# Performance work log

Hardware: AMD Instinct MI355X
Metric: run time of the kernel (lower is better)

## Reference

```python
import jax, jax.numpy as jnp
import numpy as np

N = 50000      # total nodes (25 graphs x 2000 proteins)
E = 1200000    # total edges
G = 25         # graphs
F_IN = 128     # protein_features
H = 64         # hidden_dim
L = 2          # num_layers


def setup_inputs() -> dict:
    key = jax.random.key(0)
    ks = jax.random.split(key, 24)
    inp = {
        "x": jax.random.normal(ks[0], (N, F_IN), dtype=jnp.float32),
        "edge_attr": jax.random.uniform(ks[1], (E,), dtype=jnp.float32),
        "global_features": jax.random.normal(ks[2], (G, 6), dtype=jnp.float32),
        "edge_index": jax.random.randint(ks[3], (2, E), 0, N, dtype=jnp.int64),
        "batch": (jnp.arange(N, dtype=jnp.int64) // (N // G)),
    }
    s = 0.05
    inp["W_embed"] = jax.random.normal(ks[4], (F_IN, H), dtype=jnp.float32) * s
    inp["b_embed"] = jnp.zeros((H,), dtype=jnp.float32)
    inp["W_glob"] = jax.random.normal(ks[5], (6, H), dtype=jnp.float32) * s
    inp["b_glob"] = jnp.zeros((H,), dtype=jnp.float32)
    # stacked per-layer GATConv params (heads=1)
    inp["lin_W"] = jax.random.normal(ks[6], (L, H, H), dtype=jnp.float32) * s
    inp["att_src"] = jax.random.normal(ks[7], (L, H), dtype=jnp.float32) * s
    inp["att_dst"] = jax.random.normal(ks[8], (L, H), dtype=jnp.float32) * s
    inp["lin_edge_W"] = jax.random.normal(ks[9], (L, 1, H), dtype=jnp.float32) * s
    inp["att_edge"] = jax.random.normal(ks[10], (L, H), dtype=jnp.float32) * s
    inp["gat_bias"] = jnp.zeros((L, H), dtype=jnp.float32)
    inp["W_comb"] = jax.random.normal(ks[11], (2 * H, H), dtype=jnp.float32) * s
    inp["b_comb"] = jnp.zeros((H,), dtype=jnp.float32)
    inp["W_out"] = jax.random.normal(ks[12], (H, 1), dtype=jnp.float32) * s
    inp["b_out"] = jnp.zeros((1,), dtype=jnp.float32)
    return inp


def _forward(x, edge_attr, global_features, W_embed, b_embed, W_glob, b_glob,
             lin_W, att_src, att_dst, lin_edge_W, att_edge, gat_bias,
             W_comb, b_comb, W_out, b_out, edge_index, batch):
    src, dst = edge_index[0], edge_index[1]
    h = x @ W_embed + b_embed                       # [N,H]
    g = global_features @ W_glob + b_glob           # [G,H]
    ea = edge_attr[:, None]                         # [E,1] (edge_attr.unsqueeze(1))
    for l in range(L):
        hs = h @ lin_W[l]                           # [N,H] shared lin_src/lin_dst
        a_src = hs @ att_src[l]                     # [N]
        a_dst = hs @ att_dst[l]                     # [N]
        ef = ea @ lin_edge_W[l]                     # [E,H]
        a_edge = ef @ att_edge[l]                   # [E]
        alpha = jax.nn.leaky_relu(a_src[src] + a_dst[dst] + a_edge, 0.2)
        # segment softmax over incoming edges of each dst node
        m = jax.ops.segment_max(alpha, dst, num_segments=N)
        ex = jnp.exp(alpha - m[dst])
        denom = jax.ops.segment_sum(ex, dst, num_segments=N)
        alpha = ex / (denom[dst] + 1e-16)
        msg = alpha[:, None] * hs[src]              # [E,H]
        h = jax.ops.segment_sum(msg, dst, num_segments=N) + gat_bias[l]
        h = jax.nn.relu(h)
    # global_mean_pool
    counts = jax.ops.segment_sum(jnp.ones((N,), h.dtype), batch, num_segments=G)
    graph = jax.ops.segment_sum(h, batch, num_segments=G) / counts[:, None]
    combined = jax.nn.relu(jnp.concatenate([graph, g], axis=1) @ W_comb + b_comb)
    return combined @ W_out + b_out                 # [G,1]


def reference(x, edge_attr, global_features, W_embed, b_embed, W_glob, b_glob,
              lin_W, att_src, att_dst, lin_edge_W, att_edge, gat_bias,
              W_comb, b_comb, W_out, b_out, edge_index, batch):
    return _forward(x, edge_attr, global_features, W_embed, b_embed, W_glob, b_glob,
                    lin_W, att_src, att_dst, lin_edge_W, att_edge, gat_bias,
                    W_comb, b_comb, W_out, b_out, edge_index, batch)
```

## Files before the change

kernel.cpp:

```cpp
#include <hip/hip_runtime.h>
#include <math.h>

#define N_NODES 50000
#define N_EDGES 1200000
#define N_GRAPH 25
#define F_IN 128
#define H_DIM 64
#define NODES_PER_GRAPH 2000
#define POOL_CHUNKS 32

#define NBUCK 196
#define BUCK_CAP 8000
#define EPB 4096
#define NB_BIN ((N_EDGES + EPB - 1) / EPB)

#define OFF_H     0
#define OFF_HS    (N_NODES*64)
#define OFF_ASRC  (OFF_HS + N_NODES*64)
#define OFF_ADST  (OFF_ASRC + N_NODES)
#define OFF_CBUF  (OFF_ADST + N_NODES)
#define OFF_ZERO  (OFF_CBUF + 16)
#define OFF_BCUR  OFF_ZERO
#define OFF_GSUM  (OFF_BCUR + 256)
#define OFF_ZEND  (OFF_GSUM + N_GRAPH*64)
#define OFF_BBASE OFF_ZEND
#define OFF_ROWP  (OFF_BBASE + 256)
#define OFF_ESRT  (OFF_ROWP + N_NODES + 2)

__global__ __launch_bounds__(256) void k_embed(const float* __restrict__ x,
                                               const float* __restrict__ W,
                                               const float* __restrict__ b,
                                               float* __restrict__ h) {
    int lane = threadIdx.x & 63;
    int wid0 = (blockIdx.x * 256 + threadIdx.x) >> 6;
    int nw = gridDim.x * 4;
    float wc[F_IN];
    #pragma unroll
    for (int k = 0; k < F_IN; ++k) wc[k] = W[k * H_DIM + lane];
    float bj = b[lane];
    for (int n = wid0; n < N_NODES; n += nw) {
        int nu = __builtin_amdgcn_readfirstlane(n);
        const float* row = x + (size_t)nu * F_IN;
        float acc = bj;
        #pragma unroll
        for (int k = 0; k < F_IN; ++k) acc += row[k] * wc[k];
        h[nu * H_DIM + lane] = acc;
    }
}

__global__ __launch_bounds__(256) void k_hs(const float* __restrict__ hin,
                                            const float* __restrict__ W,
                                            const float* __restrict__ attS,
                                            const float* __restrict__ attD,
                                            float* __restrict__ hs,
                                            float* __restrict__ asrc,
                                            float* __restrict__ adst) {
    int lane = threadIdx.x & 63;
    int wid0 = (blockIdx.x * 256 + threadIdx.x) >> 6;
    int nw = gridDim.x * 4;
    float wc[H_DIM];
    #pragma unroll
    for (int k = 0; k < H_DIM; ++k) wc[k] = W[k * H_DIM + lane];
    float aS = attS[lane], aD = attD[lane];
    for (int n = wid0; n < N_NODES; n += nw) {
        int nu = __builtin_amdgcn_readfirstlane(n);
        const float* row = hin + (size_t)nu * H_DIM;
        float acc = 0.f;
        #pragma unroll
        for (int k = 0; k < H_DIM; ++k) acc += row[k] * wc[k];
        hs[nu * H_DIM + lane] = acc;
        float rs = acc * aS, rd = acc * aD;
        #pragma unroll
        for (int m = 1; m < 64; m <<= 1) {
            rs += __shfl_xor(rs, m);
            rd += __shfl_xor(rd, m);
        }
        if (lane == 0) { asrc[nu] = rs; adst[nu] = rd; }
    }
}

__device__ __forceinline__ int block_excl_scan(int v, int tid, int* lds, int* total) {
    int lane = tid & 63, w = tid >> 6;
    int incl = v;
    #pragma unroll
    for (int off = 1; off < 64; off <<= 1) {
        int t = __shfl_up(incl, off);
        if (lane >= off) incl += t;
    }
    if (lane == 63) lds[w] = incl;
    __syncthreads();
    int wo = 0;
    for (int i = 0; i < w; ++i) wo += lds[i];
    *total = lds[0] + lds[1] + lds[2] + lds[3];
    __syncthreads();
    return wo + incl - v;
}

__global__ __launch_bounds__(256) void k_bin(const int* __restrict__ ei,
                                             const float* __restrict__ ea,
                                             uint2* __restrict__ stage,
                                             int* __restrict__ bcur) {
    __shared__ int lcnt[NBUCK];
    __shared__ int lbase[NBUCK];
    int tid = threadIdx.x;
    for (int i = tid; i < NBUCK; i += 256) lcnt[i] = 0;
    __syncthreads();
    int e0 = blockIdx.x * EPB;
    unsigned pw0[16], pw1[16];
    #pragma unroll
    for (int k = 0; k < 16; ++k) {
        int e = e0 + k * 256 + tid;
        bool ok = e < N_EDGES;
        int s = ok ? ei[e] : 0;
        int d = ok ? ei[N_EDGES + e] : 0;
        float v = ok ? ea[e] : 0.f;
        pw0[k] = (unsigned)s | ((unsigned)d << 16);
        pw1[k] = __float_as_uint(v);
        if (ok) atomicAdd(&lcnt[d >> 8], 1);
    }
    __syncthreads();
    for (int i = tid; i < NBUCK; i += 256) {
        lbase[i] = atomicAdd(&bcur[i], lcnt[i]);
        lcnt[i] = 0;
    }
    __syncthreads();
    #pragma unroll
    for (int k = 0; k < 16; ++k) {
        int e = e0 + k * 256 + tid;
        if (e < N_EDGES) {
            int b = pw0[k] >> 24;
            int pos = lbase[b] + atomicAdd(&lcnt[b], 1);
            uint2 t; t.x = pw0[k]; t.y = pw1[k];
            stage[b * BUCK_CAP + pos] = t;
        }
    }
}

__global__ __launch_bounds__(256) void k_bscan(const int* __restrict__ bcur,
                                               int* __restrict__ bbase,
                                               int* __restrict__ rowp,
                                               const float* __restrict__ linE,
                                               const float* __restrict__ attE,
                                               float* __restrict__ cbuf) {
    __shared__ int lds[4];
    if (threadIdx.x < 128) {
        int l = threadIdx.x >> 6, j = threadIdx.x & 63;
        float v = linE[l * 64 + j] * attE[l * 64 + j];
        #pragma unroll
        for (int m = 1; m < 64; m <<= 1) v += __shfl_xor(v, m);
        if (j == 0) cbuf[l] = v;
    }
    int v = (threadIdx.x < NBUCK) ? bcur[threadIdx.x] : 0;
    int total;
    int ex = block_excl_scan(v, threadIdx.x, lds, &total);
    if (threadIdx.x < NBUCK) bbase[threadIdx.x] = ex;
    if (threadIdx.x == 0) rowp[N_NODES] = N_EDGES;
}

__global__ __launch_bounds__(256) void k_group(const uint2* __restrict__ stage,
                                               const int* __restrict__ bcur,
                                               const int* __restrict__ bbase,
                                               int* __restrict__ rowp,
                                               unsigned* __restrict__ esrt) {
    int b = blockIdx.x;
    int tid = threadIdx.x;
    int cntb = bcur[b];
    int base = bbase[b];
    __shared__ int lcnt[256];
    __shared__ int lofs[256];
    __shared__ int slds[4];
    lcnt[tid] = 0;
    __syncthreads();
    const uint2* reg = stage + b * BUCK_CAP;
    for (int i = tid; i < cntb; i += 256)
        atomicAdd(&lcnt[(reg[i].x >> 16) & 255], 1);
    __syncthreads();
    int total;
    int ex = block_excl_scan(lcnt[tid], tid, slds, &total);
    lofs[tid] = base + ex;
    int n = b * 256 + tid;
    if (n < N_NODES) rowp[n] = base + ex;
    __syncthreads();
    lcnt[tid] = 0;
    __syncthreads();
    for (int i = tid; i < cntb; i += 256) {
        uint2 v = reg[i];
        int dloc = (v.x >> 16) & 255;
        int pos = lofs[dloc] + atomicAdd(&lcnt[dloc], 1);
        esrt[pos] = (v.x & 0xFFFFu) | ((v.y + 0x8000u) & 0xFFFF0000u);
    }
}

__global__ __launch_bounds__(256) void k_fused(const int* __restrict__ rowp,
                                               const unsigned* __restrict__ esrt,
                                               const float* __restrict__ asrc,
                                               const float* __restrict__ adst,
                                               const float* __restrict__ hs,
                                               const float* __restrict__ cbuf,
                                               int layer,
                                               const float* __restrict__ gbias,
                                               float* __restrict__ hout) {
    int wid = (blockIdx.x * 256 + threadIdx.x) >> 6;
    int lane = threadIdx.x & 63;
    if (wid >= N_NODES) return;
    int beg = rowp[wid], end = rowp[wid + 1];
    float adv = adst[wid];
    float c = cbuf[layer];
    float m = -INFINITY, sum = 0.f;
    float4 acc = make_float4(0.f, 0.f, 0.f, 0.f);
    int g = lane >> 4, fl = lane & 15;
    const float4* hs4 = (const float4*)hs;

    for (int base = beg; base < end; base += 64) {
        int idx = base + lane;
        bool ok = idx < end;
        unsigned v = ok ? esrt[idx] : 0u;
        int s = v & 0xFFFF;
        float a;
        if (ok) {
            float eav = __uint_as_float(v & 0xFFFF0000u);
            a = asrc[s] + adv + c * eav;
            a = a >= 0.f ? a : 0.2f * a;
        } else {
            a = -INFINITY;
        }
        float cm = a;
        #pragma unroll
        for (int o = 1; o < 64; o <<= 1) cm = fmaxf(cm, __shfl_xor(cm, o));
        float newm = fmaxf(m, cm);
        float scale = __expf(m - newm);
        sum *= scale;
        acc.x *= scale; acc.y *= scale; acc.z *= scale; acc.w *= scale;
        m = newm;
        float ex = ok ? __expf(a - m) : 0.f;
        float cs = ex;
        #pragma unroll
        for (int o = 1; o < 64; o <<= 1) cs += __shfl_xor(cs, o);
        sum += cs;

        int lim = end - base; if (lim > 64) lim = 64;
        int t = g;
        for (; t + 12 < lim; t += 16) {
            float w0 = __shfl(ex, t),      w1 = __shfl(ex, t + 4);
            float w2 = __shfl(ex, t + 8),  w3 = __shfl(ex, t + 12);
            int   s0 = __shfl(s, t),       s1 = __shfl(s, t + 4);
            int   s2 = __shfl(s, t + 8),   s3 = __shfl(s, t + 12);
            float4 r0 = hs4[s0 * 16 + fl];
            float4 r1 = hs4[s1 * 16 + fl];
            float4 r2 = hs4[s2 * 16 + fl];
            float4 r3 = hs4[s3 * 16 + fl];
            acc.x += w0 * r0.x; acc.y += w0 * r0.y; acc.z += w0 * r0.z; acc.w += w0 * r0.w;
            acc.x += w1 * r1.x; acc.y += w1 * r1.y; acc.z += w1 * r1.z; acc.w += w1 * r1.w;
            acc.x += w2 * r2.x; acc.y += w2 * r2.y; acc.z += w2 * r2.z; acc.w += w2 * r2.w;
            acc.x += w3 * r3.x; acc.y += w3 * r3.y; acc.z += w3 * r3.z; acc.w += w3 * r3.w;
        }
        for (; t < lim; t += 4) {
            float w0 = __shfl(ex, t);
            int   s0 = __shfl(s, t);
            float4 r0 = hs4[s0 * 16 + fl];
            acc.x += w0 * r0.x; acc.y += w0 * r0.y; acc.z += w0 * r0.z; acc.w += w0 * r0.w;
        }
    }
    acc.x += __shfl_xor(acc.x, 16); acc.y += __shfl_xor(acc.y, 16);
    acc.z += __shfl_xor(acc.z, 16); acc.w += __shfl_xor(acc.w, 16);
    acc.x += __shfl_xor(acc.x, 32); acc.y += __shfl_xor(acc.y, 32);
    acc.z += __shfl_xor(acc.z, 32); acc.w += __shfl_xor(acc.w, 32);

    if (lane < 16) {
        float inv = 1.f / (sum + 1e-16f);
        float4 gb = ((const float4*)(gbias + layer * H_DIM))[lane];
        float4 val;
        val.x = acc.x * inv + gb.x; val.x = val.x > 0.f ? val.x : 0.f;
        val.y = acc.y * inv + gb.y; val.y = val.y > 0.f ? val.y : 0.f;
        val.z = acc.z * inv + gb.z; val.z = val.z > 0.f ? val.z : 0.f;
        val.w = acc.w * inv + gb.w; val.w = val.w > 0.f ? val.w : 0.f;
        ((float4*)(hout + (size_t)wid * H_DIM))[lane] = val;
    }
}

__global__ __launch_bounds__(256) void k_pool(const float* __restrict__ h,
                                              float* __restrict__ gsum) {
    int g = blockIdx.x / POOL_CHUNKS;
    int chunk = blockIdx.x % POOL_CHUNKS;
    int wave = threadIdx.x >> 6, lane = threadIdx.x & 63;
    const int per_chunk = (NODES_PER_GRAPH + POOL_CHUNKS - 1) / POOL_CHUNKS;
    int n0 = g * NODES_PER_GRAPH + chunk * per_chunk;
    int n1 = g * NODES_PER_GRAPH + min((chunk + 1) * per_chunk, NODES_PER_GRAPH);
    float sum = 0.f;
    for (int n = n0 + wave; n < n1; n += 4)
        sum += h[(size_t)n * H_DIM + lane];
    __shared__ float spart[4][64];
    spart[wave][lane] = sum;
    __syncthreads();
    if (wave == 0) {
        float tot = spart[0][lane] + spart[1][lane] + spart[2][lane] + spart[3][lane];
        atomicAdd(gsum + g * H_DIM + lane, tot);
    }
}

__global__ __launch_bounds__(64) void k_head2(const float* __restrict__ gsum,
                                              const float* __restrict__ gf,
                                              const float* __restrict__ Wg,
                                              const float* __restrict__ bg,
                                              const float* __restrict__ Wc,
                                              const float* __restrict__ bc,
                                              const float* __restrict__ Wo,
                                              const float* __restrict__ bo,
                                              float* __restrict__ out) {
    int g = blockIdx.x;
    int lane = threadIdx.x;
    __shared__ float sgraph[64];
    __shared__ float sgf[64];
    sgraph[lane] = gsum[g * H_DIM + lane] / (float)NODES_PER_GRAPH;
    float gv = bg[lane];
    #pragma unroll
    for (int k = 0; k < 6; ++k) gv += gf[g * 6 + k] * Wg[k * 64 + lane];
    sgf[lane] = gv;
    __syncthreads();
    float cj = bc[lane];
    #pragma unroll
    for (int k = 0; k < 64; ++k) cj += sgraph[k] * Wc[k * 64 + lane];
    #pragma unroll
    for (int k = 0; k < 64; ++k) cj += sgf[k] * Wc[(64 + k) * 64 + lane];
    cj = cj > 0.f ? cj : 0.f;
    float o = cj * Wo[lane];
    #pragma unroll
    for (int m = 1; m < 64; m <<= 1) o += __shfl_xor(o, m);
    if (lane == 0) out[g] = o + bo[0];
}

extern "C" void kernel_launch(void* const* d_in, const int* in_sizes, int n_in,
                              void* d_out, int out_size, void* d_ws, size_t ws_size,
                              hipStream_t stream) {
    const float* x        = (const float*)d_in[0];
    const float* ea       = (const float*)d_in[1];
    const float* gf       = (const float*)d_in[2];
    const int*   ei       = (const int*)d_in[3];
    const float* W_embed  = (const float*)d_in[5];
    const float* b_embed  = (const float*)d_in[6];
    const float* W_glob   = (const float*)d_in[7];
    const float* b_glob   = (const float*)d_in[8];
    const float* lin_W    = (const float*)d_in[9];
    const float* att_src  = (const float*)d_in[10];
    const float* att_dst  = (const float*)d_in[11];
    const float* lin_eW   = (const float*)d_in[12];
    const float* att_edge = (const float*)d_in[13];
    const float* gat_bias = (const float*)d_in[14];
    const float* W_comb   = (const float*)d_in[15];
    const float* b_comb   = (const float*)d_in[16];
    const float* W_out    = (const float*)d_in[17];
    const float* b_out    = (const float*)d_in[18];
    float* out = (float*)d_out;
    float* ws  = (float*)d_ws;

    float*    h      = ws + OFF_H;
    float*    hs     = ws + OFF_HS;
    uint2*    stage  = (uint2*)(ws + OFF_HS);
    float*    asrc   = ws + OFF_ASRC;
    float*    adst   = ws + OFF_ADST;
    float*    cbuf   = ws + OFF_CBUF;
    int*      bcur   = (int*)(ws + OFF_BCUR);
    float*    gsum   = ws + OFF_GSUM;
    int*      bbase  = (int*)(ws + OFF_BBASE);
    int*      rowp   = (int*)(ws + OFF_ROWP);
    unsigned* esrt   = (unsigned*)(ws + OFF_ESRT);

    hipMemsetAsync(ws + OFF_ZERO, 0, (size_t)(OFF_ZEND - OFF_ZERO) * sizeof(float), stream);
    k_embed<<<2560, 256, 0, stream>>>(x, W_embed, b_embed, h);

    k_bin<<<NB_BIN, 256, 0, stream>>>(ei, ea, stage, bcur);
    k_bscan<<<1, 256, 0, stream>>>(bcur, bbase, rowp, lin_eW, att_edge, cbuf);
    k_group<<<NBUCK, 256, 0, stream>>>(stage, bcur, bbase, rowp, esrt);

    for (int l = 0; l < 2; ++l) {
        k_hs<<<2560, 256, 0, stream>>>(h, lin_W + l * 64 * 64,
                                       att_src + l * 64, att_dst + l * 64,
                                       hs, asrc, adst);
        k_fused<<<(N_NODES + 3) / 4, 256, 0, stream>>>(rowp, esrt,
                                                       asrc, adst, hs, cbuf, l,
                                                       gat_bias, h);
    }

    k_pool<<<N_GRAPH * POOL_CHUNKS, 256, 0, stream>>>(h, gsum);
    k_head2<<<N_GRAPH, 64, 0, stream>>>(gsum, gf, W_glob, b_glob,
                                        W_comb, b_comb, W_out, b_out, out);
}
```

Measured before the change: 203.9 us.

## Rewrite embed and hs GEMMs as LDS-tiled register-blocked kernels

Replaces the one-wave-per-node dot-product loops in the embedding and per-layer linear kernels with 64-node tiles. Weights and input rows are staged in shared memory, and each thread accumulates a 4x4 float4 register block. The attention dot products are now reduced with 16-lane shuffles per node. The goal is to cut redundant scalar row loads and per-node 64-lane reductions and to raise FMA density, at the cost of more LDS use per block and lower occupancy.

```diff
diff --git a/kernel.cpp b/kernel.cpp
--- a/kernel.cpp
+++ b/kernel.cpp
@@ -13,6 +13,7 @@
 #define BUCK_CAP 8000
 #define EPB 4096
 #define NB_BIN ((N_EDGES + EPB - 1) / EPB)
+#define NB_GEMM ((N_NODES + 63) / 64)
 
 #define OFF_H     0
 #define OFF_HS    (N_NODES*64)
@@ -31,20 +32,61 @@
                                                const float* __restrict__ W,
                                                const float* __restrict__ b,
                                                float* __restrict__ h) {
-    int lane = threadIdx.x & 63;
-    int wid0 = (blockIdx.x * 256 + threadIdx.x) >> 6;
-    int nw = gridDim.x * 4;
-    float wc[F_IN];
-    #pragma unroll
-    for (int k = 0; k < F_IN; ++k) wc[k] = W[k * H_DIM + lane];
-    float bj = b[lane];
-    for (int n = wid0; n < N_NODES; n += nw) {
-        int nu = __builtin_amdgcn_readfirstlane(n);
-        const float* row = x + (size_t)nu * F_IN;
-        float acc = bj;
-        #pragma unroll
-        for (int k = 0; k < F_IN; ++k) acc += row[k] * wc[k];
-        h[nu * H_DIM + lane] = acc;
+    __shared__ float4 sW4[F_IN * 16];
+    __shared__ float4 sx4[64 * 17];
+    int tid = threadIdx.x;
+    int n0 = blockIdx.x * 64;
+    const float4* W4 = (const float4*)W;
+    const float4* x4 = (const float4*)x;
+    #pragma unroll
+    for (int i = 0; i < 8; ++i) sW4[tid + i * 256] = W4[tid + i * 256];
+
+    int c4 = tid & 15, ng = tid >> 4;
+    int r = tid >> 4, q = tid & 15;
+    float4 acc[4];
+    #pragma unroll
+    for (int j = 0; j < 4; ++j) acc[j] = make_float4(0.f, 0.f, 0.f, 0.f);
+
+    for (int kh = 0; kh < 2; ++kh) {
+        __syncthreads();
+        #pragma unroll
+        for (int rb = 0; rb < 4; ++rb) {
+            int rr = r + rb * 16;
+            int n = n0 + rr;
+            float4 v = make_float4(0.f, 0.f, 0.f, 0.f);
+            if (n < N_NODES) v = x4[(size_t)n * 32 + kh * 16 + q];
+            sx4[rr * 17 + q] = v;
+        }
+        __syncthreads();
+        #pragma unroll
+        for (int kq = 0; kq < 16; ++kq) {
+            float4 wv[4];
+            #pragma unroll
+            for (int kk = 0; kk < 4; ++kk) wv[kk] = sW4[(kh * 64 + kq * 4 + kk) * 16 + c4];
+            #pragma unroll
+            for (int j = 0; j < 4; ++j) {
+                float4 xv = sx4[(ng * 4 + j) * 17 + kq];
+                float xs[4] = {xv.x, xv.y, xv.z, xv.w};
+                #pragma unroll
+                for (int kk = 0; kk < 4; ++kk) {
+                    acc[j].x = fmaf(xs[kk], wv[kk].x, acc[j].x);
+                    acc[j].y = fmaf(xs[kk], wv[kk].y, acc[j].y);
+                    acc[j].z = fmaf(xs[kk], wv[kk].z, acc[j].z);
+                    acc[j].w = fmaf(xs[kk], wv[kk].w, acc[j].w);
+                }
+            }
+        }
+    }
+    float4 bb = ((const float4*)b)[c4];
+    #pragma unroll
+    for (int j = 0; j < 4; ++j) {
+        int n = n0 + ng * 4 + j;
+        if (n < N_NODES) {
+            float4 v;
+            v.x = acc[j].x + bb.x; v.y = acc[j].y + bb.y;
+            v.z = acc[j].z + bb.z; v.w = acc[j].w + bb.w;
+            ((float4*)h)[(size_t)n * 16 + c4] = v;
+        }
     }
 }
 
@@ -55,27 +97,63 @@
                                             float* __restrict__ hs,
                                             float* __restrict__ asrc,
                                             float* __restrict__ adst) {
-    int lane = threadIdx.x & 63;
-    int wid0 = (blockIdx.x * 256 + threadIdx.x) >> 6;
-    int nw = gridDim.x * 4;
-    float wc[H_DIM];
-    #pragma unroll
-    for (int k = 0; k < H_DIM; ++k) wc[k] = W[k * H_DIM + lane];
-    float aS = attS[lane], aD = attD[lane];
-    for (int n = wid0; n < N_NODES; n += nw) {
-        int nu = __builtin_amdgcn_readfirstlane(n);
-        const float* row = hin + (size_t)nu * H_DIM;
-        float acc = 0.f;
-        #pragma unroll
-        for (int k = 0; k < H_DIM; ++k) acc += row[k] * wc[k];
-        hs[nu * H_DIM + lane] = acc;
-        float rs = acc * aS, rd = acc * aD;
-        #pragma unroll
-        for (int m = 1; m < 64; m <<= 1) {
-            rs += __shfl_xor(rs, m);
-            rd += __shfl_xor(rd, m);
-        }
-        if (lane == 0) { asrc[nu] = rs; adst[nu] = rd; }
+    __shared__ float4 sW4[H_DIM * 16];
+    __shared__ float4 sx4[64 * 17];
+    int tid = threadIdx.x;
+    int n0 = blockIdx.x * 64;
+    const float4* W4 = (const float4*)W;
+    const float4* h4 = (const float4*)hin;
+    #pragma unroll
+    for (int i = 0; i < 4; ++i) sW4[tid + i * 256] = W4[tid + i * 256];
+    int r = tid >> 4, q = tid & 15;
+    #pragma unroll
+    for (int rb = 0; rb < 4; ++rb) {
+        int rr = r + rb * 16;
+        int n = n0 + rr;
+        float4 v = make_float4(0.f, 0.f, 0.f, 0.f);
+        if (n < N_NODES) v = h4[(size_t)n * 16 + q];
+        sx4[rr * 17 + q] = v;
+    }
+    __syncthreads();
+
+    int c4 = tid & 15, ng = tid >> 4;
+    float4 acc[4];
+    #pragma unroll
+    for (int j = 0; j < 4; ++j) acc[j] = make_float4(0.f, 0.f, 0.f, 0.f);
+    #pragma unroll
+    for (int kq = 0; kq < 16; ++kq) {
+        float4 wv[4];
+        #pragma unroll
+        for (int kk = 0; kk < 4; ++kk) wv[kk] = sW4[(kq * 4 + kk) * 16 + c4];
+        #pragma unroll
+        for (int j = 0; j < 4; ++j) {
+            float4 xv = sx4[(ng * 4 + j) * 17 + kq];
+            float xs[4] = {xv.x, xv.y, xv.z, xv.w};
+            #pragma unroll
+            for (int kk = 0; kk < 4; ++kk) {
+                acc[j].x = fmaf(xs[kk], wv[kk].x, acc[j].x);
+                acc[j].y = fmaf(xs[kk], wv[kk].y, acc[j].y);
+                acc[j].z = fmaf(xs[kk], wv[kk].z, acc[j].z);
+                acc[j].w = fmaf(xs[kk], wv[kk].w, acc[j].w);
+            }
+        }
+    }
+    float4 aS = ((const float4*)attS)[c4];
+    float4 aD = ((const float4*)attD)[c4];
+    #pragma unroll
+    for (int j = 0; j < 4; ++j) {
+        int n = n0 + ng * 4 + j;
+        float rs = acc[j].x * aS.x + acc[j].y * aS.y + acc[j].z * aS.z + acc[j].w * aS.w;
+        float rd = acc[j].x * aD.x + acc[j].y * aD.y + acc[j].z * aD.z + acc[j].w * aD.w;
+        #pragma unroll
+        for (int o = 1; o < 16; o <<= 1) {
+            rs += __shfl_xor(rs, o);
+            rd += __shfl_xor(rd, o);
+        }
+        if (n < N_NODES) {
+            ((float4*)hs)[(size_t)n * 16 + c4] = acc[j];
+            if (c4 == 0) { asrc[n] = rs; adst[n] = rd; }
+        }
     }
 }
 
@@ -366,16 +444,16 @@
     unsigned* esrt   = (unsigned*)(ws + OFF_ESRT);
 
     hipMemsetAsync(ws + OFF_ZERO, 0, (size_t)(OFF_ZEND - OFF_ZERO) * sizeof(float), stream);
-    k_embed<<<2560, 256, 0, stream>>>(x, W_embed, b_embed, h);
+    k_embed<<<NB_GEMM, 256, 0, stream>>>(x, W_embed, b_embed, h);
 
     k_bin<<<NB_BIN, 256, 0, stream>>>(ei, ea, stage, bcur);
     k_bscan<<<1, 256, 0, stream>>>(bcur, bbase, rowp, lin_eW, att_edge, cbuf);
     k_group<<<NBUCK, 256, 0, stream>>>(stage, bcur, bbase, rowp, esrt);
 
     for (int l = 0; l < 2; ++l) {
-        k_hs<<<2560, 256, 0, stream>>>(h, lin_W + l * 64 * 64,
-                                       att_src + l * 64, att_dst + l * 64,
-                                       hs, asrc, adst);
+        k_hs<<<NB_GEMM, 256, 0, stream>>>(h, lin_W + l * 64 * 64,
+                                          att_src + l * 64, att_dst + l * 64,
+                                          hs, asrc, adst);
         k_fused<<<(N_NODES + 3) / 4, 256, 0, stream>>>(rowp, esrt,
                                                        asrc, adst, hs, cbuf, l,
                                                        gat_bias, h);
```

Measured after the change: 215.8 us. 5.8% more time.
